# Performance work log

Measured on AMD Instinct MI355X. Metric: run time of the kernel, lower is better.

The kernel has to match this reference:

```python
import jax, jax.numpy as jnp
import numpy as np

N_NODES = 100000
N_EDGES = 1600000
IN_DIM = 128
HID = 128
OUT = 128
NUM_GRAPHS = 2048


def setup_inputs() -> dict:
    key = jax.random.key(0)
    ks = jax.random.split(key, 10)
    x = jax.random.normal(ks[0], (N_NODES, IN_DIM), dtype=jnp.float32)
    edge_index = jax.random.randint(ks[1], (2, N_EDGES), 0, N_NODES, dtype=jnp.int32)
    graph_index = jnp.sort(jax.random.randint(ks[2], (N_NODES,), 0, NUM_GRAPHS, dtype=jnp.int32))
    def glorot(k, fi, fo):
        lim = jnp.sqrt(6.0 / (fi + fo)).astype(jnp.float32)
        return jax.random.uniform(k, (fi, fo), jnp.float32, -lim, lim)
    return {
        "x": x,
        "edge_index": edge_index,
        "graph_index": graph_index,
        "num_graphs": NUM_GRAPHS,
        "W1": glorot(ks[3], IN_DIM, HID), "b1": jnp.zeros((HID,), jnp.float32),
        "W2": glorot(ks[4], HID, HID),    "b2": jnp.zeros((HID,), jnp.float32),
        "W3": glorot(ks[5], HID, OUT),    "b3": jnp.zeros((OUT,), jnp.float32),
    }


def _gcn_layer(x, src, dst, norm, W, b, n_nodes):
    # transform first (cheap GEMM), then normalized gather-scatter aggregation
    h = x @ W                              # [N, F]
    msg = h[src] * norm[:, None]           # [E+N, F] gather + scale
    out = jax.ops.segment_sum(msg, dst, num_segments=n_nodes)  # scatter-add
    return out + b


def reference(x, edge_index, graph_index, num_graphs, W1, b1, W2, b2, W3, b3):
    n = x.shape[0]
    # add self-loops (PyG GCNConv default)
    loops = jnp.arange(n, dtype=edge_index.dtype)
    src = jnp.concatenate([edge_index[0], loops])
    dst = jnp.concatenate([edge_index[1], loops])
    # symmetric normalization D^-1/2 (A+I) D^-1/2, degree = in-degree incl. self-loop
    deg = jax.ops.segment_sum(jnp.ones_like(src, dtype=x.dtype), dst, num_segments=n)
    dinv = jax.lax.rsqrt(jnp.maximum(deg, 1.0))
    norm = dinv[src] * dinv[dst]
    # 3 conv layers + ReLU (dropout = identity at inference)
    h = jax.nn.relu(_gcn_layer(x, src, dst, norm, W1, b1, n))
    h = jax.nn.relu(_gcn_layer(h, src, dst, norm, W2, b2, n))
    h = jax.nn.relu(_gcn_layer(h, src, dst, norm, W3, b3, n))
    # global mean / max pooling per graph
    gsum = jax.ops.segment_sum(h, graph_index, num_segments=num_graphs)
    cnt = jax.ops.segment_sum(jnp.ones((n,), h.dtype), graph_index, num_segments=num_graphs)
    gmean = gsum / jnp.maximum(cnt, 1.0)[:, None]
    gmax = jax.ops.segment_max(h, graph_index, num_segments=num_graphs)
    return jnp.concatenate([gmean, gmax], axis=-1)
```

## Files before the change

kernel.cpp:

```cpp
#include <hip/hip_runtime.h>
#include <hip/hip_bf16.h>
#include <stdint.h>

#define N_NODES   100000
#define N_EDGES   1600000
#define FDIM      128
#define NUM_GR    2048
#define CSR_CAP   64

#define NBKT      391
#define BKT_CAP   4864
#define TILE      4096
#define LBIN_CAP  32
#define LBIN_STR  33

typedef __attribute__((ext_vector_type(8))) short short8;
typedef __attribute__((ext_vector_type(4))) float f32x4;

__device__ __forceinline__ uint32_t pk2(float a, float b) {
    __hip_bfloat16 x = __float2bfloat16(a), y = __float2bfloat16(b);
    uint16_t ux = *reinterpret_cast<uint16_t*>(&x);
    uint16_t uy = *reinterpret_cast<uint16_t*>(&y);
    return (uint32_t)ux | ((uint32_t)uy << 16);
}

__device__ __forceinline__ float bflo(uint32_t u) { return __uint_as_float(u << 16); }
__device__ __forceinline__ float bfhi(uint32_t u) { return __uint_as_float(u & 0xFFFF0000u); }


__global__ __launch_bounds__(256) void k_bucket_wprep(
        const int* __restrict__ src, const int* __restrict__ dst,
        int* __restrict__ bkt_cnt, int* __restrict__ bkt, int E, int gA,
        const float* __restrict__ W1, const float* __restrict__ W2,
        const float* __restrict__ W3, __hip_bfloat16* __restrict__ wt) {
    int b = blockIdx.x;
    if (b >= gA) {
        int idx = (b - gA) * 256 + threadIdx.x;
        int l = idx >> 14, rem = idx & 16383, c = rem >> 7, k = rem & 127;
        const float* W = (l == 0) ? W1 : ((l == 1) ? W2 : W3);
        wt[idx] = __float2bfloat16(W[k * FDIM + c]);
        return;
    }

    __shared__ int binCnt[NBKT];
    __shared__ int binBase[NBKT];
    __shared__ int bins[NBKT * LBIN_STR];

    for (int i = threadIdx.x; i < NBKT; i += 256) binCnt[i] = 0;
    __syncthreads();

    int e0 = b * TILE;
    int e1 = min(E, e0 + TILE);
    for (int e = e0 + threadIdx.x; e < e1; e += 256) {
        int s = src[e];
        int d = dst[e];
        int bi = d >> 8;
        int rec = ((d & 255) << 17) | s;
        int pos = atomicAdd(&binCnt[bi], 1);
        if (pos < LBIN_CAP) {
            bins[bi * LBIN_STR + pos] = rec;
        } else {
            int gp = atomicAdd(&bkt_cnt[bi], 1);
            if (gp < BKT_CAP) bkt[bi * BKT_CAP + gp] = rec;
        }
    }
    __syncthreads();

    for (int i = threadIdx.x; i < NBKT; i += 256) {
        int c = min(binCnt[i], LBIN_CAP);
        binBase[i] = (c > 0) ? atomicAdd(&bkt_cnt[i], c) : 0;
    }
    __syncthreads();

    for (int i = threadIdx.x; i < NBKT * LBIN_CAP; i += 256) {
        int bi = i / LBIN_CAP, sl = i - bi * LBIN_CAP;
        if (sl < min(binCnt[bi], LBIN_CAP)) {
            int gp = binBase[bi] + sl;
            if (gp < BKT_CAP) bkt[bi * BKT_CAP + gp] = bins[bi * LBIN_STR + sl];
        }
    }
}


__global__ __launch_bounds__(256) void k_csr(const int* __restrict__ bkt_cnt,
                                             const int* __restrict__ bkt,
                                             int* __restrict__ cnt,
                                             float* __restrict__ dinv,
                                             int* __restrict__ csr, int n) {
    __shared__ int lc[256];
    __shared__ int cur[256];
    int b = blockIdx.x;
    int tid = threadIdx.x;
    lc[tid] = 0;
    cur[tid] = 0;
    __syncthreads();

    int len = min(bkt_cnt[b], BKT_CAP);
    const int* recs = bkt + b * BKT_CAP;

    for (int i = tid; i < len; i += 256)
        atomicAdd(&lc[(recs[i] >> 17) & 255], 1);
    __syncthreads();

    int v = (b << 8) + tid;
    if (v < n) {
        int c = lc[tid];
        cnt[v] = c;
        dinv[v] = rsqrtf((float)(c + 1));
    }

    for (int i = tid; i < len; i += 256) {
        int rec = recs[i];
        int dl = (rec >> 17) & 255;
        int pos = atomicAdd(&cur[dl], 1);
        if (pos < CSR_CAP)
            csr[(((size_t)(b << 8) + dl) << 6) + pos] = rec & 0x1FFFF;
    }
}


template<bool AF32>
__global__ __launch_bounds__(256) void k_gemm(const void* __restrict__ Ap,
                                              const __hip_bfloat16* __restrict__ Wt,
                                              const float* __restrict__ dinv,
                                              __hip_bfloat16* __restrict__ C, int n) {
    __shared__ uint32_t lds[2 * 128 * 64];
    uint32_t* Atl = lds;
    uint32_t* Wtl = lds + 128 * 64;

    const int tid = threadIdx.x;
    const int rowBase = blockIdx.x * 128;

    if constexpr (AF32) {
        const float* A = (const float*)Ap;
        for (int it = 0; it < 16; ++it) {
            int g = it * 256 + tid;
            int r = g >> 5;
            int seg = g & 31;
            float4 v = make_float4(0.f, 0.f, 0.f, 0.f);
            if (rowBase + r < n) v = *(const float4*)&A[(size_t)(rowBase + r) * FDIM + seg * 4];
            int gg = seg >> 1;
            int word = r * 64 + (((gg ^ (r & 7)) << 2) | ((seg & 1) << 1));
            uint2 pv;
            pv.x = pk2(v.x, v.y);
            pv.y = pk2(v.z, v.w);
            *(uint2*)&Atl[word] = pv;
        }
    } else {
        const uint4* A4 = (const uint4*)Ap;
        for (int it = 0; it < 8; ++it) {
            int g = it * 256 + tid;
            int r = g >> 4;
            int seg = g & 15;
            uint4 v = make_uint4(0, 0, 0, 0);
            if (rowBase + r < n) v = A4[((size_t)rowBase + r) * 16 + seg];
            int word = r * 64 + ((seg ^ (r & 7)) << 2);
            *(uint4*)&Atl[word] = v;
        }
    }
    for (int it = 0; it < 8; ++it) {
        int g = it * 256 + tid;
        int r = g >> 4;
        int seg = g & 15;
        uint4 v = *(const uint4*)&Wt[(size_t)r * FDIM + seg * 8];
        int word = r * 64 + ((seg ^ (r & 7)) << 2);
        *(uint4*)&Wtl[word] = v;
    }
    __syncthreads();

    const int w = tid >> 6;
    const int lane = tid & 63;
    const int r = lane & 15;
    const int q = lane >> 4;

    f32x4 acc[8][2] = {};

#pragma unroll
    for (int kk = 0; kk < 4; ++kk) {
        int gr = ((kk * 4 + q) ^ (r & 7)) << 2;
        short8 a0 = *(const short8*)&Atl[(w * 32 + r) * 64 + gr];
        short8 a1 = *(const short8*)&Atl[(w * 32 + 16 + r) * 64 + gr];
#pragma unroll
        for (int m = 0; m < 8; ++m) {
            short8 bw = *(const short8*)&Wtl[(m * 16 + r) * 64 + gr];
            acc[m][0] = __builtin_amdgcn_mfma_f32_16x16x32_bf16(bw, a0, acc[m][0], 0, 0, 0);
            acc[m][1] = __builtin_amdgcn_mfma_f32_16x16x32_bf16(bw, a1, acc[m][1], 0, 0, 0);
        }
    }

#pragma unroll
    for (int nt = 0; nt < 2; ++nt) {
        int node = rowBase + w * 32 + nt * 16 + r;
        if (node < n) {
            float dv = dinv[node];
#pragma unroll
            for (int m = 0; m < 8; ++m) {
                f32x4 v = acc[m][nt];
                uint2 pv;
                pv.x = pk2(v[0] * dv, v[1] * dv);
                pv.y = pk2(v[2] * dv, v[3] * dv);
                *(uint2*)&C[(size_t)node * FDIM + m * 16 + q * 4] = pv;
            }
        }
    }
}


__global__ __launch_bounds__(256) void k_agg(const __hip_bfloat16* __restrict__ T,
                                             const int* __restrict__ cnt,
                                             const int* __restrict__ csr,
                                             const float* __restrict__ dinv,
                                             const float* __restrict__ bias,
                                             uint32_t* __restrict__ Hb,
                                             int n) {
    int wid = (blockIdx.x * 256 + threadIdx.x) >> 6;
    int lane = threadIdx.x & 63;
    if (wid >= n) return;
    int v = wid;
    int g   = lane >> 4;
    int s16 = lane & 15;

    const uint4* Tu4 = (const uint4*)T;

    int cv  = min(cnt[v], CSR_CAP);
    int sraw = csr[((size_t)v << 6) + lane];
    int sidx = (lane < cv) ? sraw : ((lane == cv) ? v : n);
    cv += 1;

    float a0 = 0.f, a1 = 0.f, a2 = 0.f, a3 = 0.f;
    float a4 = 0.f, a5 = 0.f, a6 = 0.f, a7 = 0.f;

    int mr = (cv + 15) & ~15;
    for (int j = 0; j < mr; j += 16) {
        uint4 gg[4];
#pragma unroll
        for (int t = 0; t < 4; ++t) {
            int it = __shfl(sidx, j + 4 * t + g, 64);
            gg[t] = Tu4[(size_t)it * 16 + s16];
        }
#pragma unroll
        for (int t = 0; t < 4; ++t) {
            a0 += bflo(gg[t].x); a1 += bfhi(gg[t].x);
            a2 += bflo(gg[t].y); a3 += bfhi(gg[t].y);
            a4 += bflo(gg[t].z); a5 += bfhi(gg[t].z);
            a6 += bflo(gg[t].w); a7 += bfhi(gg[t].w);
        }
    }

    a0 += __shfl_xor(a0, 16, 64); a0 += __shfl_xor(a0, 32, 64);
    a1 += __shfl_xor(a1, 16, 64); a1 += __shfl_xor(a1, 32, 64);
    a2 += __shfl_xor(a2, 16, 64); a2 += __shfl_xor(a2, 32, 64);
    a3 += __shfl_xor(a3, 16, 64); a3 += __shfl_xor(a3, 32, 64);
    a4 += __shfl_xor(a4, 16, 64); a4 += __shfl_xor(a4, 32, 64);
    a5 += __shfl_xor(a5, 16, 64); a5 += __shfl_xor(a5, 32, 64);
    a6 += __shfl_xor(a6, 16, 64); a6 += __shfl_xor(a6, 32, 64);
    a7 += __shfl_xor(a7, 16, 64); a7 += __shfl_xor(a7, 32, 64);

    if (g == 0) {
        float dv = dinv[v];
        float4 bb0 = *(const float4*)&bias[s16 * 8];
        float4 bb1 = *(const float4*)&bias[s16 * 8 + 4];
        float r0 = fmaxf(fmaf(dv, a0, bb0.x), 0.f);
        float r1 = fmaxf(fmaf(dv, a1, bb0.y), 0.f);
        float r2 = fmaxf(fmaf(dv, a2, bb0.z), 0.f);
        float r3 = fmaxf(fmaf(dv, a3, bb0.w), 0.f);
        float r4 = fmaxf(fmaf(dv, a4, bb1.x), 0.f);
        float r5 = fmaxf(fmaf(dv, a5, bb1.y), 0.f);
        float r6 = fmaxf(fmaf(dv, a6, bb1.z), 0.f);
        float r7 = fmaxf(fmaf(dv, a7, bb1.w), 0.f);
        uint4 pv;
        pv.x = pk2(r0, r1);
        pv.y = pk2(r2, r3);
        pv.z = pk2(r4, r5);
        pv.w = pk2(r6, r7);
        *(uint4*)&Hb[(size_t)v * 64 + s16 * 4] = pv;
    }
}


__device__ __forceinline__ int lower_bound_dev(const int* a, int n, int key) {
    int lo = 0, hi = n;
    while (lo < hi) {
        int m = (lo + hi) >> 1;
        if (a[m] < key) lo = m + 1; else hi = m;
    }
    return lo;
}

__global__ __launch_bounds__(256) void k_pool2(const uint32_t* __restrict__ Hb,
                                               const int* __restrict__ gidx,
                                               float* __restrict__ out, int n) {
    __shared__ float ls0[256], ls1[256], lm0[256], lm1[256];
    int g = blockIdx.x;
    int w = threadIdx.x >> 6;
    int lane = threadIdx.x & 63;

    int lo = lower_bound_dev(gidx, n, g);
    int hi = lower_bound_dev(gidx, n, g + 1);

    float s0 = 0.f, s1 = 0.f, m0 = 0.f, m1 = 0.f;
    for (int v = lo + w; v < hi; v += 4) {
        uint32_t u = Hb[(size_t)v * 64 + lane];
        float x0 = bflo(u), x1 = bfhi(u);
        s0 += x0; s1 += x1;
        m0 = fmaxf(m0, x0); m1 = fmaxf(m1, x1);
    }
    ls0[threadIdx.x] = s0; ls1[threadIdx.x] = s1;
    lm0[threadIdx.x] = m0; lm1[threadIdx.x] = m1;
    __syncthreads();

    if (w == 0) {
#pragma unroll
        for (int ww = 1; ww < 4; ++ww) {
            s0 += ls0[ww * 64 + lane]; s1 += ls1[ww * 64 + lane];
            m0 = fmaxf(m0, lm0[ww * 64 + lane]);
            m1 = fmaxf(m1, lm1[ww * 64 + lane]);
        }
        float inv = 1.f / (float)max(hi - lo, 1);
        float* og = out + (size_t)g * 2 * FDIM;
        og[lane * 2]     = s0 * inv;
        og[lane * 2 + 1] = s1 * inv;
        og[FDIM + lane * 2]     = m0;
        og[FDIM + lane * 2 + 1] = m1;
    }
}


extern "C" void kernel_launch(void* const* d_in, const int* in_sizes, int n_in,
                              void* d_out, int out_size, void* d_ws, size_t ws_size,
                              hipStream_t stream) {
    const float* x    = (const float*)d_in[0];
    const int*   ei   = (const int*)d_in[1];
    const int*   gidx = (const int*)d_in[2];
    const float* W1 = (const float*)d_in[4];
    const float* b1 = (const float*)d_in[5];
    const float* W2 = (const float*)d_in[6];
    const float* b2 = (const float*)d_in[7];
    const float* W3 = (const float*)d_in[8];
    const float* b3 = (const float*)d_in[9];
    float* out = (float*)d_out;

    const int N = N_NODES, E = N_EDGES;
    const int* src = ei;
    const int* dst = ei + E;

    char* ws = (char*)d_ws;
    size_t o = 0;
    auto alloc = [&](size_t bytes) { size_t r = o; o += (bytes + 255) & ~(size_t)255; return r; };
    size_t o_bktcnt = alloc((size_t)NBKT * 4);
    size_t o_bkt    = alloc((size_t)NBKT * BKT_CAP * 4);
    size_t o_cnt    = alloc((size_t)N * 4);
    size_t o_dinv   = alloc((size_t)N * 4);
    size_t o_csr    = alloc((size_t)NBKT * 256 * CSR_CAP * 4);
    size_t o_wt     = alloc((size_t)3 * FDIM * FDIM * 2);
    size_t o_t      = alloc((size_t)(N + 1) * FDIM * 2);
    size_t o_h      = alloc((size_t)N * FDIM * 2);

    int*   bkt_cnt = (int*)(ws + o_bktcnt);
    int*   bkt     = (int*)(ws + o_bkt);
    int*   cnt     = (int*)(ws + o_cnt);
    float* dinv    = (float*)(ws + o_dinv);
    int*   csr     = (int*)(ws + o_csr);
    __hip_bfloat16* wtbuf = (__hip_bfloat16*)(ws + o_wt);
    __hip_bfloat16* tbuf  = (__hip_bfloat16*)(ws + o_t);
    __hip_bfloat16* hb16  = (__hip_bfloat16*)(ws + o_h);

    hipMemsetAsync(bkt_cnt, 0, (size_t)NBKT * 4, stream);
    hipMemsetAsync(tbuf + (size_t)N * FDIM, 0, FDIM * 2, stream);

    const int gA = (E + TILE - 1) / TILE;

    k_bucket_wprep<<<gA + 192, 256, 0, stream>>>(src, dst, bkt_cnt, bkt, E, gA,
                                                 W1, W2, W3, wtbuf);
    k_csr<<<NBKT, 256, 0, stream>>>(bkt_cnt, bkt, cnt, dinv, csr, N);

    const int gGemm = (N + 127) / 128;
    const int gAgg  = (N + 3) / 4;

    k_gemm<true><<<gGemm, 256, 0, stream>>>(x, wtbuf, dinv, tbuf, N);
    k_agg<<<gAgg, 256, 0, stream>>>(tbuf, cnt, csr, dinv, b1, (uint32_t*)hb16, N);
    k_gemm<false><<<gGemm, 256, 0, stream>>>(hb16, wtbuf + FDIM * FDIM, dinv, tbuf, N);
    k_agg<<<gAgg, 256, 0, stream>>>(tbuf, cnt, csr, dinv, b2, (uint32_t*)hb16, N);
    k_gemm<false><<<gGemm, 256, 0, stream>>>(hb16, wtbuf + 2 * FDIM * FDIM, dinv, tbuf, N);
    k_agg<<<gAgg, 256, 0, stream>>>(tbuf, cnt, csr, dinv, b3, (uint32_t*)hb16, N);

    k_pool2<<<NUM_GR, 256, 0, stream>>>((const uint32_t*)hb16, gidx, out, N);
}
```

Before: 409.2 us.

## Fuse layer-1 GEMM with edge bucketing and move dinv scaling into aggregation

The first-layer GEMM no longer needs dinv, so it now runs inside the same launch as edge bucketing and weight prep, with the source-side dinv weight applied per gathered edge in a weighted aggregation variant. This removes a dependency and one kernel launch, letting the GEMM overlap with the atomics-heavy bucketing. The CSR build is split into four blocks per bucket for more parallelism, at the cost of each block rereading the whole bucket. The weighted aggregation adds one extra scalar gather of dinv per edge, and a padding dinv entry is set to zero for the dummy index.

```diff
diff --git a/kernel.cpp b/kernel.cpp
--- a/kernel.cpp
+++ b/kernel.cpp
@@ -28,55 +28,128 @@
 __device__ __forceinline__ float bfhi(uint32_t u) { return __uint_as_float(u & 0xFFFF0000u); }
 
 
-__global__ __launch_bounds__(256) void k_bucket_wprep(
+__global__ __launch_bounds__(256) void k_fused1(
+        const float* __restrict__ x, const float* __restrict__ W1,
+        __hip_bfloat16* __restrict__ C, int n, int gGemm,
         const int* __restrict__ src, const int* __restrict__ dst,
         int* __restrict__ bkt_cnt, int* __restrict__ bkt, int E, int gA,
-        const float* __restrict__ W1, const float* __restrict__ W2,
-        const float* __restrict__ W3, __hip_bfloat16* __restrict__ wt) {
-    int b = blockIdx.x;
-    if (b >= gA) {
-        int idx = (b - gA) * 256 + threadIdx.x;
+        const float* __restrict__ W2, const float* __restrict__ W3,
+        __hip_bfloat16* __restrict__ wt) {
+    __shared__ uint32_t smem[16384];
+    const int b = blockIdx.x;
+    const int tid = threadIdx.x;
+
+    if (b >= gGemm + gA) {
+        int idx = 16384 + (b - gGemm - gA) * 256 + tid;
         int l = idx >> 14, rem = idx & 16383, c = rem >> 7, k = rem & 127;
-        const float* W = (l == 0) ? W1 : ((l == 1) ? W2 : W3);
+        const float* W = (l == 1) ? W2 : W3;
         wt[idx] = __float2bfloat16(W[k * FDIM + c]);
         return;
     }
 
-    __shared__ int binCnt[NBKT];
-    __shared__ int binBase[NBKT];
-    __shared__ int bins[NBKT * LBIN_STR];
-
-    for (int i = threadIdx.x; i < NBKT; i += 256) binCnt[i] = 0;
+    if (b >= gGemm) {
+        int* binCnt  = (int*)smem;
+        int* binBase = (int*)smem + NBKT;
+        int* bins    = (int*)smem + 2 * NBKT;
+        int bb = b - gGemm;
+
+        for (int i = tid; i < NBKT; i += 256) binCnt[i] = 0;
+        __syncthreads();
+
+        int e0 = bb * TILE;
+        int e1 = min(E, e0 + TILE);
+        for (int e = e0 + tid; e < e1; e += 256) {
+            int s = src[e];
+            int d = dst[e];
+            int bi = d >> 8;
+            int rec = ((d & 255) << 17) | s;
+            int pos = atomicAdd(&binCnt[bi], 1);
+            if (pos < LBIN_CAP) {
+                bins[bi * LBIN_STR + pos] = rec;
+            } else {
+                int gp = atomicAdd(&bkt_cnt[bi], 1);
+                if (gp < BKT_CAP) bkt[bi * BKT_CAP + gp] = rec;
+            }
+        }
+        __syncthreads();
+
+        for (int i = tid; i < NBKT; i += 256) {
+            int c = min(binCnt[i], LBIN_CAP);
+            binBase[i] = (c > 0) ? atomicAdd(&bkt_cnt[i], c) : 0;
+        }
+        __syncthreads();
+
+        for (int i = tid; i < NBKT * LBIN_CAP; i += 256) {
+            int bi = i / LBIN_CAP, sl = i - bi * LBIN_CAP;
+            if (sl < min(binCnt[bi], LBIN_CAP)) {
+                int gp = binBase[bi] + sl;
+                if (gp < BKT_CAP) bkt[bi * BKT_CAP + gp] = bins[bi * LBIN_STR + sl];
+            }
+        }
+        return;
+    }
+
+    uint32_t* Atl = smem;
+    uint32_t* Wtl = smem + 128 * 64;
+
+    const int rowBase = b * 128;
+
+    for (int it = 0; it < 16; ++it) {
+        int g = it * 256 + tid;
+        int r = g >> 5;
+        int seg = g & 31;
+        float4 v = make_float4(0.f, 0.f, 0.f, 0.f);
+        if (rowBase + r < n) v = *(const float4*)&x[(size_t)(rowBase + r) * FDIM + seg * 4];
+        int gg = seg >> 1;
+        int word = r * 64 + (((gg ^ (r & 7)) << 2) | ((seg & 1) << 1));
+        uint2 pv;
+        pv.x = pk2(v.x, v.y);
+        pv.y = pk2(v.z, v.w);
+        *(uint2*)&Atl[word] = pv;
+    }
+    for (int it = 0; it < 32; ++it) {
+        int idx = it * 256 + tid;
+        int kp = idx >> 7;
+        int c  = idx & 127;
+        float w0 = W1[(size_t)(2 * kp) * FDIM + c];
+        float w1 = W1[(size_t)(2 * kp + 1) * FDIM + c];
+        int word = c * 64 + ((((kp >> 2) ^ (c & 7)) << 2) | (kp & 3));
+        Wtl[word] = pk2(w0, w1);
+    }
     __syncthreads();
 
-    int e0 = b * TILE;
-    int e1 = min(E, e0 + TILE);
-    for (int e = e0 + threadIdx.x; e < e1; e += 256) {
-        int s = src[e];
-        int d = dst[e];
-        int bi = d >> 8;
-        int rec = ((d & 255) << 17) | s;
-        int pos = atomicAdd(&binCnt[bi], 1);
-        if (pos < LBIN_CAP) {
-            bins[bi * LBIN_STR + pos] = rec;
-        } else {
-            int gp = atomicAdd(&bkt_cnt[bi], 1);
-            if (gp < BKT_CAP) bkt[bi * BKT_CAP + gp] = rec;
-        }
-    }
-    __syncthreads();
-
-    for (int i = threadIdx.x; i < NBKT; i += 256) {
-        int c = min(binCnt[i], LBIN_CAP);
-        binBase[i] = (c > 0) ? atomicAdd(&bkt_cnt[i], c) : 0;
-    }
-    __syncthreads();
-
-    for (int i = threadIdx.x; i < NBKT * LBIN_CAP; i += 256) {
-        int bi = i / LBIN_CAP, sl = i - bi * LBIN_CAP;
-        if (sl < min(binCnt[bi], LBIN_CAP)) {
-            int gp = binBase[bi] + sl;
-            if (gp < BKT_CAP) bkt[bi * BKT_CAP + gp] = bins[bi * LBIN_STR + sl];
+    const int w = tid >> 6;
+    const int lane = tid & 63;
+    const int r = lane & 15;
+    const int q = lane >> 4;
+
+    f32x4 acc[8][2] = {};
+
+#pragma unroll
+    for (int kk = 0; kk < 4; ++kk) {
+        int gr = ((kk * 4 + q) ^ (r & 7)) << 2;
+        short8 a0 = *(const short8*)&Atl[(w * 32 + r) * 64 + gr];
+        short8 a1 = *(const short8*)&Atl[(w * 32 + 16 + r) * 64 + gr];
+#pragma unroll
+        for (int m = 0; m < 8; ++m) {
+            short8 bw = *(const short8*)&Wtl[(m * 16 + r) * 64 + gr];
+            acc[m][0] = __builtin_amdgcn_mfma_f32_16x16x32_bf16(bw, a0, acc[m][0], 0, 0, 0);
+            acc[m][1] = __builtin_amdgcn_mfma_f32_16x16x32_bf16(bw, a1, acc[m][1], 0, 0, 0);
+        }
+    }
+
+#pragma unroll
+    for (int nt = 0; nt < 2; ++nt) {
+        int node = rowBase + w * 32 + nt * 16 + r;
+        if (node < n) {
+#pragma unroll
+            for (int m = 0; m < 8; ++m) {
+                f32x4 v = acc[m][nt];
+                uint2 pv;
+                pv.x = pk2(v[0], v[1]);
+                pv.y = pk2(v[2], v[3]);
+                *(uint2*)&C[(size_t)node * FDIM + m * 16 + q * 4] = pv;
+            }
         }
     }
 }
@@ -87,40 +160,49 @@
                                              int* __restrict__ cnt,
                                              float* __restrict__ dinv,
                                              int* __restrict__ csr, int n) {
-    __shared__ int lc[256];
-    __shared__ int cur[256];
+    __shared__ int lc[64];
+    __shared__ int cur[64];
     int b = blockIdx.x;
     int tid = threadIdx.x;
-    lc[tid] = 0;
-    cur[tid] = 0;
+    int bi = b >> 2;
+    int qd = b & 3;
+
+    if (b == 0 && tid == 0) dinv[n] = 0.f;
+
+    if (tid < 64) { lc[tid] = 0; cur[tid] = 0; }
     __syncthreads();
 
-    int len = min(bkt_cnt[b], BKT_CAP);
-    const int* recs = bkt + b * BKT_CAP;
-
-    for (int i = tid; i < len; i += 256)
-        atomicAdd(&lc[(recs[i] >> 17) & 255], 1);
+    int len = min(bkt_cnt[bi], BKT_CAP);
+    const int* recs = bkt + bi * BKT_CAP;
+
+    for (int i = tid; i < len; i += 256) {
+        int dl = (recs[i] >> 17) & 255;
+        if ((dl >> 6) == qd) atomicAdd(&lc[dl & 63], 1);
+    }
     __syncthreads();
 
-    int v = (b << 8) + tid;
-    if (v < n) {
-        int c = lc[tid];
-        cnt[v] = c;
-        dinv[v] = rsqrtf((float)(c + 1));
+    if (tid < 64) {
+        int v = (bi << 8) + (qd << 6) + tid;
+        if (v < n) {
+            int c = lc[tid];
+            cnt[v] = c;
+            dinv[v] = rsqrtf((float)(c + 1));
+        }
     }
 
     for (int i = tid; i < len; i += 256) {
         int rec = recs[i];
         int dl = (rec >> 17) & 255;
-        int pos = atomicAdd(&cur[dl], 1);
-        if (pos < CSR_CAP)
-            csr[(((size_t)(b << 8) + dl) << 6) + pos] = rec & 0x1FFFF;
-    }
-}
-
-
-template<bool AF32>
-__global__ __launch_bounds__(256) void k_gemm(const void* __restrict__ Ap,
+        if ((dl >> 6) == qd) {
+            int pos = atomicAdd(&cur[dl & 63], 1);
+            if (pos < CSR_CAP)
+                csr[(((size_t)(bi << 8) + dl) << 6) + pos] = rec & 0x1FFFF;
+        }
+    }
+}
+
+
+__global__ __launch_bounds__(256) void k_gemm(const __hip_bfloat16* __restrict__ Ap,
                                               const __hip_bfloat16* __restrict__ Wt,
                                               const float* __restrict__ dinv,
                                               __hip_bfloat16* __restrict__ C, int n) {
@@ -131,32 +213,15 @@
     const int tid = threadIdx.x;
     const int rowBase = blockIdx.x * 128;
 
-    if constexpr (AF32) {
-        const float* A = (const float*)Ap;
-        for (int it = 0; it < 16; ++it) {
-            int g = it * 256 + tid;
-            int r = g >> 5;
-            int seg = g & 31;
-            float4 v = make_float4(0.f, 0.f, 0.f, 0.f);
-            if (rowBase + r < n) v = *(const float4*)&A[(size_t)(rowBase + r) * FDIM + seg * 4];
-            int gg = seg >> 1;
-            int word = r * 64 + (((gg ^ (r & 7)) << 2) | ((seg & 1) << 1));
-            uint2 pv;
-            pv.x = pk2(v.x, v.y);
-            pv.y = pk2(v.z, v.w);
-            *(uint2*)&Atl[word] = pv;
-        }
-    } else {
-        const uint4* A4 = (const uint4*)Ap;
-        for (int it = 0; it < 8; ++it) {
-            int g = it * 256 + tid;
-            int r = g >> 4;
-            int seg = g & 15;
-            uint4 v = make_uint4(0, 0, 0, 0);
-            if (rowBase + r < n) v = A4[((size_t)rowBase + r) * 16 + seg];
-            int word = r * 64 + ((seg ^ (r & 7)) << 2);
-            *(uint4*)&Atl[word] = v;
-        }
+    const uint4* A4 = (const uint4*)Ap;
+    for (int it = 0; it < 8; ++it) {
+        int g = it * 256 + tid;
+        int r = g >> 4;
+        int seg = g & 15;
+        uint4 v = make_uint4(0, 0, 0, 0);
+        if (rowBase + r < n) v = A4[((size_t)rowBase + r) * 16 + seg];
+        int word = r * 64 + ((seg ^ (r & 7)) << 2);
+        *(uint4*)&Atl[word] = v;
     }
     for (int it = 0; it < 8; ++it) {
         int g = it * 256 + tid;
@@ -206,6 +271,7 @@
 }
 
 
+template<int WEIGHTED>
 __global__ __launch_bounds__(256) void k_agg(const __hip_bfloat16* __restrict__ T,
                                              const int* __restrict__ cnt,
                                              const int* __restrict__ csr,
@@ -233,17 +299,26 @@
     int mr = (cv + 15) & ~15;
     for (int j = 0; j < mr; j += 16) {
         uint4 gg[4];
+        float wv[4];
 #pragma unroll
         for (int t = 0; t < 4; ++t) {
             int it = __shfl(sidx, j + 4 * t + g, 64);
+            if constexpr (WEIGHTED) wv[t] = dinv[it];
             gg[t] = Tu4[(size_t)it * 16 + s16];
         }
 #pragma unroll
         for (int t = 0; t < 4; ++t) {
-            a0 += bflo(gg[t].x); a1 += bfhi(gg[t].x);
-            a2 += bflo(gg[t].y); a3 += bfhi(gg[t].y);
-            a4 += bflo(gg[t].z); a5 += bfhi(gg[t].z);
-            a6 += bflo(gg[t].w); a7 += bfhi(gg[t].w);
+            if constexpr (WEIGHTED) {
+                a0 = fmaf(wv[t], bflo(gg[t].x), a0); a1 = fmaf(wv[t], bfhi(gg[t].x), a1);
+                a2 = fmaf(wv[t], bflo(gg[t].y), a2); a3 = fmaf(wv[t], bfhi(gg[t].y), a3);
+                a4 = fmaf(wv[t], bflo(gg[t].z), a4); a5 = fmaf(wv[t], bfhi(gg[t].z), a5);
+                a6 = fmaf(wv[t], bflo(gg[t].w), a6); a7 = fmaf(wv[t], bfhi(gg[t].w), a7);
+            } else {
+                a0 += bflo(gg[t].x); a1 += bfhi(gg[t].x);
+                a2 += bflo(gg[t].y); a3 += bfhi(gg[t].y);
+                a4 += bflo(gg[t].z); a5 += bfhi(gg[t].z);
+                a6 += bflo(gg[t].w); a7 += bfhi(gg[t].w);
+            }
         }
     }
 
@@ -350,7 +425,7 @@
     size_t o_bktcnt = alloc((size_t)NBKT * 4);
     size_t o_bkt    = alloc((size_t)NBKT * BKT_CAP * 4);
     size_t o_cnt    = alloc((size_t)N * 4);
-    size_t o_dinv   = alloc((size_t)N * 4);
+    size_t o_dinv   = alloc((size_t)(N + 1) * 4);
     size_t o_csr    = alloc((size_t)NBKT * 256 * CSR_CAP * 4);
     size_t o_wt     = alloc((size_t)3 * FDIM * FDIM * 2);
     size_t o_t      = alloc((size_t)(N + 1) * FDIM * 2);
@@ -368,21 +443,21 @@
     hipMemsetAsync(bkt_cnt, 0, (size_t)NBKT * 4, stream);
     hipMemsetAsync(tbuf + (size_t)N * FDIM, 0, FDIM * 2, stream);
 
-    const int gA = (E + TILE - 1) / TILE;
-
-    k_bucket_wprep<<<gA + 192, 256, 0, stream>>>(src, dst, bkt_cnt, bkt, E, gA,
-                                                 W1, W2, W3, wtbuf);
-    k_csr<<<NBKT, 256, 0, stream>>>(bkt_cnt, bkt, cnt, dinv, csr, N);
-
+    const int gA    = (E + TILE - 1) / TILE;
     const int gGemm = (N + 127) / 128;
-    const int gAgg  = (N + 3) / 4;
-
-    k_gemm<true><<<gGemm, 256, 0, stream>>>(x, wtbuf, dinv, tbuf, N);
-    k_agg<<<gAgg, 256, 0, stream>>>(tbuf, cnt, csr, dinv, b1, (uint32_t*)hb16, N);
-    k_gemm<false><<<gGemm, 256, 0, stream>>>(hb16, wtbuf + FDIM * FDIM, dinv, tbuf, N);
-    k_agg<<<gAgg, 256, 0, stream>>>(tbuf, cnt, csr, dinv, b2, (uint32_t*)hb16, N);
-    k_gemm<false><<<gGemm, 256, 0, stream>>>(hb16, wtbuf + 2 * FDIM * FDIM, dinv, tbuf, N);
-    k_agg<<<gAgg, 256, 0, stream>>>(tbuf, cnt, csr, dinv, b3, (uint32_t*)hb16, N);
+
+    k_fused1<<<gGemm + gA + 128, 256, 0, stream>>>(x, W1, tbuf, N, gGemm,
+                                                   src, dst, bkt_cnt, bkt, E, gA,
+                                                   W2, W3, wtbuf);
+    k_csr<<<NBKT * 4, 256, 0, stream>>>(bkt_cnt, bkt, cnt, dinv, csr, N);
+
+    const int gAgg = (N + 3) / 4;
+
+    k_agg<1><<<gAgg, 256, 0, stream>>>(tbuf, cnt, csr, dinv, b1, (uint32_t*)hb16, N);
+    k_gemm<<<gGemm, 256, 0, stream>>>(hb16, wtbuf + FDIM * FDIM, dinv, tbuf, N);
+    k_agg<0><<<gAgg, 256, 0, stream>>>(tbuf, cnt, csr, dinv, b2, (uint32_t*)hb16, N);
+    k_gemm<<<gGemm, 256, 0, stream>>>(hb16, wtbuf + 2 * FDIM * FDIM, dinv, tbuf, N);
+    k_agg<0><<<gAgg, 256, 0, stream>>>(tbuf, cnt, csr, dinv, b3, (uint32_t*)hb16, N);
 
     k_pool2<<<NUM_GR, 256, 0, stream>>>((const uint32_t*)hb16, gidx, out, N);
 }
```

Measured after the change: 403.5 us. No clear change (-1.4%).
